# Optimization experiments

Measured on AMD Instinct MI355X. Metric: run time of the kernel, lower is better.

Reference implementation:

```python
import jax, jax.numpy as jnp
import numpy as np

DIM = 2048
NUM_HEADS = 16
HEAD_DIM = DIM // NUM_HEADS
FF_MULT = 2
ROPE_BASE = 10000.0
EPS = 1e-6


def _rmsnorm(x, g):
    return x * jax.lax.rsqrt(jnp.mean(x * x, axis=-1, keepdims=True) + EPS) * g


def _rope_tables(seq_len):
    half = HEAD_DIM // 2
    inv_freq = 1.0 / (ROPE_BASE ** (2.0 * jnp.arange(half, dtype=jnp.float32) / HEAD_DIM))
    angles = jnp.arange(seq_len, dtype=jnp.float32)[:, None] * inv_freq[None, :]  # (S, half)
    return jnp.cos(angles), jnp.sin(angles)


def _apply_rope(x, cos, sin):
    # x: (B, H, S, D); cos/sin: (S, D/2). Interleaved pairs (RoFormer form).
    x_even = x[..., 0::2]
    x_odd = x[..., 1::2]
    c = cos[None, None].astype(x.dtype)
    s = sin[None, None].astype(x.dtype)
    rot_even = x_even * c - x_odd * s
    rot_odd = x_odd * c + x_even * s
    return jnp.stack([rot_even, rot_odd], axis=-1).reshape(x.shape)


def setup_inputs() -> dict:
    key = jax.random.key(0)
    ks = jax.random.split(key, 7)
    B, S = 2, 2048
    scale = 1.0 / np.sqrt(DIM)
    return {
        "x": jax.random.normal(ks[0], (B, S, DIM), dtype=jnp.float32),
        "w_qkv": jax.random.normal(ks[1], (DIM, 3 * DIM), dtype=jnp.float32) * scale,
        "w_out": jax.random.normal(ks[2], (DIM, DIM), dtype=jnp.float32) * scale,
        "w_fc": jax.random.normal(ks[3], (DIM, DIM * FF_MULT), dtype=jnp.float32) * scale,
        "w_proj": jax.random.normal(ks[4], (DIM * FF_MULT, DIM), dtype=jnp.float32) / np.sqrt(DIM * FF_MULT),
        "g_in": jnp.ones((DIM,), dtype=jnp.float32),
        "g_ff": jnp.ones((DIM,), dtype=jnp.float32),
    }


def reference(x, w_qkv, w_out, w_fc, w_proj, g_in, g_ff):
    B, S, D = x.shape
    # --- attention branch ---
    h = _rmsnorm(x, g_in)
    qkv = h @ w_qkv  # (B, S, 3D)
    q, k, v = jnp.split(qkv, 3, axis=-1)
    def heads(t):
        return t.reshape(B, S, NUM_HEADS, HEAD_DIM).transpose(0, 2, 1, 3)
    q, k, v = heads(q), heads(k), heads(v)  # (B, H, S, Dh)
    cos, sin = _rope_tables(S)
    q = _apply_rope(q, cos, sin)
    k = _apply_rope(k, cos, sin)
    scores = jnp.einsum("bhqd,bhkd->bhqk", q, k) / jnp.asarray(np.sqrt(HEAD_DIM), x.dtype)
    causal = jnp.tril(jnp.ones((S, S), dtype=bool))
    scores = jnp.where(causal[None, None], scores, jnp.asarray(-jnp.inf, scores.dtype))
    attn = jax.nn.softmax(scores, axis=-1)
    out = jnp.einsum("bhqk,bhkd->bhqd", attn, v)  # (B, H, S, Dh)
    out = out.transpose(0, 2, 1, 3).reshape(B, S, D)
    x = x + out @ w_out
    # --- feed-forward branch ---
    h = _rmsnorm(x, g_ff)
    x = x + jax.nn.gelu(h @ w_fc) @ w_proj
    return x


if __name__ == "__main__":
    inp = setup_inputs()
    y = reference(**inp)
    print(y.shape, y.dtype)
```

## Files before the change

kernel.cpp:

```cpp
#include <hip/hip_runtime.h>
#include <math.h>

typedef __bf16 bf16x8 __attribute__((ext_vector_type(8)));
typedef __bf16 bf16x4 __attribute__((ext_vector_type(4)));
typedef __bf16 bf16x2 __attribute__((ext_vector_type(2)));
typedef float  f32x4  __attribute__((ext_vector_type(4)));

#define DEV __device__ __forceinline__

DEV void gload16(const void* g, void* l) {
  __builtin_amdgcn_global_load_lds(
      (const __attribute__((address_space(1))) void*)g,
      (__attribute__((address_space(3))) void*)l, 16, 0, 0);
}

__global__ __launch_bounds__(256) void transpose_cvt(
    const float* __restrict__ in, __bf16* __restrict__ outT, int R, int C) {
  __shared__ float t[64][65];
  const int c0 = blockIdx.x * 64, r0 = blockIdx.y * 64;
  const int tid = threadIdx.x;
#pragma unroll
  for (int i = 0; i < 4; i++) {
    int r = (tid >> 4) + i * 16;
    int cf = tid & 15;
    float4 v = *(const float4*)(in + (size_t)(r0 + r) * C + c0 + cf * 4);
    t[r][cf * 4 + 0] = v.x; t[r][cf * 4 + 1] = v.y;
    t[r][cf * 4 + 2] = v.z; t[r][cf * 4 + 3] = v.w;
  }
  __syncthreads();
#pragma unroll
  for (int i = 0; i < 2; i++) {
    int c = (tid >> 3) + i * 32;
    int r8 = tid & 7;
    bf16x8 ov;
#pragma unroll
    for (int k = 0; k < 8; k++) ov[k] = (__bf16)t[r8 * 8 + k][c];
    *(bf16x8*)(outT + (size_t)(c0 + c) * R + r0 + r8 * 8) = ov;
  }
}

__global__ __launch_bounds__(256) void rmsnorm_kernel(
    const float* __restrict__ x, const float* __restrict__ g, __bf16* __restrict__ out) {
  const int r = blockIdx.x, t = threadIdx.x;
  const float4* xr = (const float4*)(x + (size_t)r * 2048);
  float4 a = xr[2 * t], b = xr[2 * t + 1];
  float ss = a.x * a.x + a.y * a.y + a.z * a.z + a.w * a.w +
             b.x * b.x + b.y * b.y + b.z * b.z + b.w * b.w;
#pragma unroll
  for (int mk = 1; mk < 64; mk <<= 1) ss += __shfl_xor(ss, mk);
  __shared__ float red[4];
  if ((t & 63) == 0) red[t >> 6] = ss;
  __syncthreads();
  const float sc = rsqrtf((red[0] + red[1] + red[2] + red[3]) * (1.0f / 2048.0f) + 1e-6f);
  const float4* gr = (const float4*)g;
  float4 ga = gr[2 * t], gb = gr[2 * t + 1];
  bf16x8 ov;
  ov[0] = (__bf16)(a.x * sc * ga.x); ov[1] = (__bf16)(a.y * sc * ga.y);
  ov[2] = (__bf16)(a.z * sc * ga.z); ov[3] = (__bf16)(a.w * sc * ga.w);
  ov[4] = (__bf16)(b.x * sc * gb.x); ov[5] = (__bf16)(b.y * sc * gb.y);
  ov[6] = (__bf16)(b.z * sc * gb.z); ov[7] = (__bf16)(b.w * sc * gb.w);
  *(bf16x8*)(out + (size_t)r * 2048 + t * 8) = ov;
}

template <int EPI>
__global__ __launch_bounds__(256) void gemm_bt(
    const __bf16* __restrict__ A, const __bf16* __restrict__ BT,
    void* __restrict__ Cout, const float* __restrict__ res, int M, int N, int K) {
  __shared__ char lds[32768];
  char* As = lds;
  char* Bs = lds + 16384;
  const int tid = threadIdx.x;
  const int lane = tid & 63;
  const int bn = blockIdx.x, bm = blockIdx.y;
  const int wm = tid >> 7, wn = (tid >> 6) & 1;

  f32x4 acc[4][4];
#pragma unroll
  for (int i = 0; i < 4; i++)
#pragma unroll
    for (int j = 0; j < 4; j++) acc[i][j] = (f32x4){0.f, 0.f, 0.f, 0.f};

  const size_t strideA = (size_t)K * 2;
  const char* ga[4];
  const char* gb[4];
#pragma unroll
  for (int t = 0; t < 4; t++) {
    int gg = t * 256 + tid;
    int row = gg >> 3, slot = gg & 7;
    ga[t] = (const char*)A + (size_t)(bm * 128 + row) * strideA + ((slot ^ (row & 7)) << 4);
    gb[t] = (const char*)BT + (size_t)(bn * 128 + row) * strideA + ((slot ^ (row & 7)) << 4);
  }

  for (int k0 = 0; k0 < K; k0 += 64) {
    __syncthreads();
#pragma unroll
    for (int t = 0; t < 4; t++) {
      int gg = t * 256 + tid;
      gload16(ga[t], As + gg * 16);
      gload16(gb[t], Bs + gg * 16);
      ga[t] += 128;
      gb[t] += 128;
    }
    __syncthreads();
#pragma unroll
    for (int kk = 0; kk < 2; kk++) {
      bf16x8 a[4], b[4];
      const int c16 = kk * 4 + (lane >> 4);
#pragma unroll
      for (int i = 0; i < 4; i++) {
        int ra = wm * 64 + i * 16 + (lane & 15);
        a[i] = *(const bf16x8*)(As + ra * 128 + ((c16 ^ (ra & 7)) << 4));
        int rb = wn * 64 + i * 16 + (lane & 15);
        b[i] = *(const bf16x8*)(Bs + rb * 128 + ((c16 ^ (rb & 7)) << 4));
      }
#pragma unroll
      for (int i = 0; i < 4; i++)
#pragma unroll
        for (int j = 0; j < 4; j++)
          acc[i][j] = __builtin_amdgcn_mfma_f32_16x16x32_bf16(a[i], b[j], acc[i][j], 0, 0, 0);
    }
  }

#pragma unroll
  for (int i = 0; i < 4; i++)
#pragma unroll
    for (int j = 0; j < 4; j++)
#pragma unroll
      for (int r = 0; r < 4; r++) {
        int row = bm * 128 + wm * 64 + i * 16 + ((lane >> 4) << 2) + r;
        int col = bn * 128 + wn * 64 + j * 16 + (lane & 15);
        size_t idx = (size_t)row * N + col;
        float v = acc[i][j][r];
        if (EPI == 0) {
          ((__bf16*)Cout)[idx] = (__bf16)v;
        } else if (EPI == 1) {
          ((float*)Cout)[idx] = v + res[idx];
        } else {
          float u = 0.7978845608028654f * (v + 0.044715f * v * v * v);
          ((__bf16*)Cout)[idx] = (__bf16)(0.5f * v * (1.0f + tanhf(u)));
        }
      }
}

__global__ __launch_bounds__(256, 6) void gemm_qkv(
    const __bf16* __restrict__ A, const __bf16* __restrict__ BT,
    __bf16* __restrict__ qr, __bf16* __restrict__ kr, __bf16* __restrict__ vt,
    int K) {
  __shared__ char lds[32768];
  char* As = lds;
  char* Bs = lds + 16384;
  const int tid = threadIdx.x;
  const int lane = tid & 63;
  const int bn = blockIdx.x, bm = blockIdx.y;
  const int wm = tid >> 7, wn = (tid >> 6) & 1;

  f32x4 acc[4][4];
#pragma unroll
  for (int i = 0; i < 4; i++)
#pragma unroll
    for (int j = 0; j < 4; j++) acc[i][j] = (f32x4){0.f, 0.f, 0.f, 0.f};

  const size_t strideA = (size_t)K * 2;
  const char* ga[4];
  const char* gb[4];
#pragma unroll
  for (int t = 0; t < 4; t++) {
    int gg = t * 256 + tid;
    int row = gg >> 3, slot = gg & 7;
    ga[t] = (const char*)A + (size_t)(bm * 128 + row) * strideA + ((slot ^ (row & 7)) << 4);
    gb[t] = (const char*)BT + (size_t)(bn * 128 + row) * strideA + ((slot ^ (row & 7)) << 4);
  }

  for (int k0 = 0; k0 < K; k0 += 64) {
    __syncthreads();
#pragma unroll
    for (int t = 0; t < 4; t++) {
      int gg = t * 256 + tid;
      gload16(ga[t], As + gg * 16);
      gload16(gb[t], Bs + gg * 16);
      ga[t] += 128;
      gb[t] += 128;
    }
    __syncthreads();
#pragma unroll
    for (int kk = 0; kk < 2; kk++) {
      bf16x8 a[4], b[4];
      const int c16 = kk * 4 + (lane >> 4);
#pragma unroll
      for (int i = 0; i < 4; i++) {
        int ra = wm * 64 + i * 16 + (lane & 15);
        a[i] = *(const bf16x8*)(As + ra * 128 + ((c16 ^ (ra & 7)) << 4));
        int rb = wn * 64 + i * 16 + (lane & 15);
        b[i] = *(const bf16x8*)(Bs + rb * 128 + ((c16 ^ (rb & 7)) << 4));
      }
#pragma unroll
      for (int i = 0; i < 4; i++)
#pragma unroll
        for (int j = 0; j < 4; j++)
          acc[i][j] = __builtin_amdgcn_mfma_f32_16x16x32_bf16(a[i], b[j], acc[i][j], 0, 0, 0);
    }
  }

  const int colbase = bn * 128 + wn * 64;
  if (bn < 32) {
#pragma unroll
    for (int j = 0; j < 4; j++) {
      int col = colbase + j * 16 + (lane & 15);
      int isK = col >> 11;
      int hh = (col >> 7) & 15, d = col & 127;
      float invr = exp2f(-0.20762050593045952f * (float)(d >> 1)) *
                   0.15915494309189535f;
      __bf16* dst = isK ? kr : qr;
#pragma unroll
      for (int i = 0; i < 4; i++)
#pragma unroll
        for (int r = 0; r < 4; r++) {
          int row = bm * 128 + wm * 64 + i * 16 + ((lane >> 4) << 2) + r;
          int bb = row >> 11, srel = row & 2047;
          float me = acc[i][j][r];
          float pv = __shfl_xor(me, 1);
          if (!(lane & 1)) {
            float ar = (float)srel * invr;
            ar = ar - floorf(ar);
            float cs = __builtin_amdgcn_cosf(ar);
            float sn = __builtin_amdgcn_sinf(ar);
            bf16x2 pk;
            pk[0] = (__bf16)(me * cs - pv * sn);
            pk[1] = (__bf16)(pv * cs + me * sn);
            *(bf16x2*)(dst + ((size_t)((bb * 16 + hh) * 2048 + srel)) * 128 + d) = pk;
          }
        }
    }
  } else {
#pragma unroll
    for (int i = 0; i < 4; i++)
#pragma unroll
      for (int j = 0; j < 4; j++) {
        int col = colbase + j * 16 + (lane & 15) - 4096;
        int hh = col >> 7, d = col & 127;
        int row0 = bm * 128 + wm * 64 + i * 16 + ((lane >> 4) << 2);
        int bb = row0 >> 11, srel = row0 & 2047;
        bf16x4 pk;
#pragma unroll
        for (int r = 0; r < 4; r++) pk[r] = (__bf16)acc[i][j][r];
        *(bf16x4*)(vt + ((size_t)((bb * 16 + hh) * 128 + d)) * 2048 + srel) = pk;
      }
  }
}

#define MMQ(IB, JB, AR, BR)                                                   \
  __builtin_amdgcn_s_setprio(1);                                              \
  _Pragma("unroll") for (int i = 0; i < 4; i++)                               \
      _Pragma("unroll") for (int j = 0; j < 2; j++)                           \
          _Pragma("unroll") for (int kk = 0; kk < 2; kk++)                    \
              acc[(IB)*4 + i][(JB)*2 + j] =                                   \
      __builtin_amdgcn_mfma_f32_16x16x32_bf16(                                \
          AR[i][kk], BR[j][kk], acc[(IB)*4 + i][(JB)*2 + j], 0, 0, 0);        \
  __builtin_amdgcn_s_setprio(0);

template <int EPI>
__global__ __launch_bounds__(512, 2) void gemm256(
    const __bf16* __restrict__ A, const __bf16* __restrict__ BT,
    void* __restrict__ Cout, const float* __restrict__ res, int M, int N, int K) {
  __shared__ char lds[131072];
  const int tid = threadIdx.x, lane = tid & 63, w = tid >> 6;
  const int wm = w >> 2, wn = w & 3;
  const int bn = blockIdx.x, bm = blockIdx.y;

  f32x4 acc[8][4];
#pragma unroll
  for (int i = 0; i < 8; i++)
#pragma unroll
    for (int j = 0; j < 4; j++) acc[i][j] = (f32x4){0.f, 0.f, 0.f, 0.f};

  const size_t strideA = (size_t)K * 2;
  const int r0 = tid >> 3, s0 = tid & 7;
  const int r1 = r0 + 64;
  const char* Ab0 = (const char*)A + (size_t)(bm * 256) * strideA;
  const char* Bb0 = (const char*)BT + (size_t)(bn * 256) * strideA;

  auto stage = [&](int isB, int h, int kt, int buf) {
    const char* g = (isB ? Bb0 : Ab0) + (size_t)(h * 128) * strideA + (size_t)kt * 128;
    char* d = lds + isB * 65536 + buf * 32768 + h * 16384;
    gload16(g + (size_t)r0 * strideA + ((s0 ^ (r0 & 7)) << 4), d + tid * 16);
    gload16(g + (size_t)r1 * strideA + ((s0 ^ (r1 & 7)) << 4), d + (tid + 512) * 16);
  };
  auto ldA = [&](bf16x8 (&a)[4][2], int buf, int bank) {
    const char* base = lds + buf * 32768 + wm * 16384;
#pragma unroll
    for (int i = 0; i < 4; i++)
#pragma unroll
      for (int kk = 0; kk < 2; kk++) {
        int rl = bank * 64 + i * 16 + (lane & 15);
        int c16 = kk * 4 + (lane >> 4);
        a[i][kk] = *(const bf16x8*)(base + rl * 128 + ((c16 ^ (rl & 7)) << 4));
      }
  };
  auto ldB = [&](bf16x8 (&b)[2][2], int buf, int jb) {
    const char* base = lds + 65536 + buf * 32768 + (wn >> 1) * 16384;
#pragma unroll
    for (int j = 0; j < 2; j++)
#pragma unroll
      for (int kk = 0; kk < 2; kk++) {
        int rl = (wn & 1) * 64 + jb * 32 + j * 16 + (lane & 15);
        int c16 = kk * 4 + (lane >> 4);
        b[j][kk] = *(const bf16x8*)(base + rl * 128 + ((c16 ^ (rl & 7)) << 4));
      }
  };

  const int NT = K >> 6;
  stage(1, 0, 0, 0); stage(1, 1, 0, 0); stage(0, 0, 0, 0); stage(0, 1, 0, 0);
  stage(1, 0, 1, 1); stage(1, 1, 1, 1); stage(0, 0, 1, 1); stage(0, 1, 1, 1);
  asm volatile("s_waitcnt vmcnt(6)" ::: "memory");
  __builtin_amdgcn_s_barrier();

  bf16x8 a[4][2], b0[2][2], b1[2][2];
  for (int it = 0; it < (NT >> 1); ++it) {
    const int e = 2 * it;
    const int ep = (e + 2 < NT) ? e + 2 : NT - 1;
    const int op = (e + 3 < NT) ? e + 3 : NT - 1;
    ldA(a, 0, 0); ldB(b0, 0, 0);
    __builtin_amdgcn_s_barrier();
    MMQ(0, 0, a, b0);
    __builtin_amdgcn_s_barrier();
    ldB(b1, 0, 1);
    __builtin_amdgcn_s_barrier();
    MMQ(0, 1, a, b1);
    __builtin_amdgcn_s_barrier();
    ldA(a, 0, 1); stage(1, 0, ep, 0);
    __builtin_amdgcn_s_barrier();
    MMQ(1, 1, a, b1);
    __builtin_amdgcn_s_barrier();
    stage(1, 1, ep, 0);
    asm volatile("s_waitcnt vmcnt(4)" ::: "memory");
    __builtin_amdgcn_s_barrier();
    MMQ(1, 0, a, b0);
    __builtin_amdgcn_s_barrier();
    ldA(a, 1, 0); ldB(b0, 1, 0); stage(0, 0, ep, 0);
    __builtin_amdgcn_s_barrier();
    MMQ(0, 0, a, b0);
    __builtin_amdgcn_s_barrier();
    ldB(b1, 1, 1); stage(0, 1, ep, 0);
    __builtin_amdgcn_s_barrier();
    MMQ(0, 1, a, b1);
    __builtin_amdgcn_s_barrier();
    ldA(a, 1, 1); stage(1, 0, op, 1);
    __builtin_amdgcn_s_barrier();
    MMQ(1, 1, a, b1);
    __builtin_amdgcn_s_barrier();
    stage(1, 1, op, 1); stage(0, 0, op, 1); stage(0, 1, op, 1);
    asm volatile("s_waitcnt vmcnt(6)" ::: "memory");
    __builtin_amdgcn_s_barrier();
    MMQ(1, 0, a, b0);
    __builtin_amdgcn_s_barrier();
  }
  asm volatile("s_waitcnt vmcnt(0)" ::: "memory");

#pragma unroll
  for (int i = 0; i < 8; i++)
#pragma unroll
    for (int j = 0; j < 4; j++)
#pragma unroll
      for (int r = 0; r < 4; r++) {
        int row = bm * 256 + wm * 128 + i * 16 + ((lane >> 4) << 2) + r;
        int col = bn * 256 + wn * 64 + j * 16 + (lane & 15);
        size_t idx = (size_t)row * N + col;
        float v = acc[i][j][r];
        if (EPI == 0) {
          ((__bf16*)Cout)[idx] = (__bf16)v;
        } else if (EPI == 1) {
          ((float*)Cout)[idx] = v + res[idx];
        } else {
          float u = 0.7978845608028654f * (v + 0.044715f * v * v * v);
          ((__bf16*)Cout)[idx] = (__bf16)(0.5f * v * (1.0f + tanhf(u)));
        }
      }
}

__global__ __launch_bounds__(512) void flash_attn(
    const __bf16* __restrict__ qg, const __bf16* __restrict__ kg,
    const __bf16* __restrict__ vtg, __bf16* __restrict__ og) {
  __shared__ char lds[81920];
  const int tid = threadIdx.x, lane = tid & 63, w = tid >> 6;
  const int h = blockIdx.y, b = blockIdx.z;
  const int bh = b * 16 + h;
  const __bf16* qb = qg + (size_t)bh * 2048 * 128;
  const char* kbb = (const char*)(kg + (size_t)bh * 2048 * 128);
  const char* vbb = (const char*)(vtg + (size_t)bh * 128 * 2048);
  char* Pw = lds + 65536 + w * 2048;

  const char* gK[2];
  const char* gV[2];
#pragma unroll
  for (int t = 0; t < 2; t++) {
    int gg = t * 512 + tid;
    int rk = gg >> 4, sk = gg & 15;
    gK[t] = kbb + rk * 256 + ((sk ^ (rk & 15)) << 4);
    int rv = gg >> 3, sv = gg & 7;
    gV[t] = vbb + rv * 4096 + ((sv ^ (rv & 7)) << 4);
  }

  const float SL2E = 0.08838834764831845f * 1.4426950408889634f;

  auto stageKV = [&](int kt, int buf) {
#pragma unroll
    for (int t = 0; t < 2; t++) {
      int gg = t * 512 + tid;
      gload16(gK[t] + (size_t)kt * 16384, lds + buf * 16384 + gg * 16);
      gload16(gV[t] + (size_t)kt * 128, lds + 32768 + buf * 16384 + gg * 16);
    }
  };

  auto run_qtile = [&](int qt) {
    const int qrow0 = qt * 128 + w * 16;
    bf16x8 qf[4];
#pragma unroll
    for (int c = 0; c < 4; c++) {
      bf16x8 raw = *(const bf16x8*)(qb + (size_t)(qrow0 + (lane & 15)) * 128 +
                                    c * 32 + ((lane >> 4) << 3));
#pragma unroll
      for (int e = 0; e < 8; e++) qf[c][e] = (__bf16)((float)raw[e] * SL2E);
    }
    float m[4], lsp[4];
    f32x4 o[8];
#pragma unroll
    for (int r = 0; r < 4; r++) { m[r] = -__builtin_inff(); lsp[r] = 0.f; }
#pragma unroll
    for (int n = 0; n < 8; n++) o[n] = (f32x4){0.f, 0.f, 0.f, 0.f};

    const int NKT = 2 * qt + 2;
    stageKV(0, 0);

    for (int kt = 0; kt < NKT; kt++) {
      const int cur = kt & 1;
      const char* Ks = lds + cur * 16384;
      const char* Vs = lds + 32768 + cur * 16384;
      if (kt < NKT - 1) {
        stageKV(kt + 1, cur ^ 1);
        asm volatile("s_waitcnt vmcnt(4)" ::: "memory");
      } else {
        asm volatile("s_waitcnt vmcnt(0)" ::: "memory");
      }
      __builtin_amdgcn_s_barrier();

      f32x4 s[4];
      __builtin_amdgcn_s_setprio(1);
#pragma unroll
      for (int n = 0; n < 4; n++) {
        s[n] = (f32x4){0.f, 0.f, 0.f, 0.f};
#pragma unroll
        for (int c = 0; c < 4; c++) {
          int krow = n * 16 + (lane & 15);
          int c16 = c * 4 + (lane >> 4);
          bf16x8 kf = *(const bf16x8*)(Ks + krow * 256 + ((c16 ^ (krow & 15)) << 4));
          s[n] = __builtin_amdgcn_mfma_f32_16x16x32_bf16(qf[c], kf, s[n], 0, 0, 0);
        }
      }
      __builtin_amdgcn_s_setprio(0);

      if (kt * 64 + 63 > qrow0) {
#pragma unroll
        for (int r = 0; r < 4; r++) {
          const int qrow = qrow0 + ((lane >> 4) << 2) + r;
#pragma unroll
          for (int n = 0; n < 4; n++) {
            int col = kt * 64 + n * 16 + (lane & 15);
            if (col > qrow) s[n][r] = -__builtin_inff();
          }
        }
      }

      float tmx[4];
#pragma unroll
      for (int r = 0; r < 4; r++)
        tmx[r] = fmaxf(fmaxf(s[0][r], s[1][r]), fmaxf(s[2][r], s[3][r]));
      bool hot = (tmx[0] > m[0] + 8.f) | (tmx[1] > m[1] + 8.f) |
                 (tmx[2] > m[2] + 8.f) | (tmx[3] > m[3] + 8.f);
      if (__any(hot)) {
        float fc[4];
#pragma unroll
        for (int r = 0; r < 4; r++) {
          float gmx = tmx[r];
#pragma unroll
          for (int mk = 1; mk < 16; mk <<= 1) gmx = fmaxf(gmx, __shfl_xor(gmx, mk));
          float nm = fmaxf(m[r], gmx);
          fc[r] = __builtin_amdgcn_exp2f(m[r] - nm);
          m[r] = nm;
          lsp[r] *= fc[r];
        }
#pragma unroll
        for (int n = 0; n < 8; n++) {
          o[n][0] *= fc[0]; o[n][1] *= fc[1]; o[n][2] *= fc[2]; o[n][3] *= fc[3];
        }
      }

      float p[4][4];
#pragma unroll
      for (int r = 0; r < 4; r++) {
        float sum = 0.f;
#pragma unroll
        for (int n = 0; n < 4; n++) {
          float pv = __builtin_amdgcn_exp2f(s[n][r] - m[r]);
          p[n][r] = pv;
          sum += pv;
        }
        lsp[r] += sum;
      }

#pragma unroll
      for (int n = 0; n < 4; n++)
#pragma unroll
        for (int r = 0; r < 4; r++) {
          int prow = ((lane >> 4) << 2) + r;
          int col = n * 16 + (lane & 15);
          int ch = col >> 3;
          *(__bf16*)(Pw + prow * 128 + ((ch ^ (prow & 7)) << 4) + ((col & 7) << 1)) =
              (__bf16)p[n][r];
        }

      __builtin_amdgcn_s_setprio(1);
#pragma unroll
      for (int kk = 0; kk < 2; kk++) {
        int prow = lane & 15;
        int pc = kk * 4 + (lane >> 4);
        bf16x8 pf = *(const bf16x8*)(Pw + prow * 128 + ((pc ^ (prow & 7)) << 4));
#pragma unroll
        for (int n = 0; n < 8; n++) {
          int vr = n * 16 + (lane & 15);
          bf16x8 vf = *(const bf16x8*)(Vs + vr * 128 + ((pc ^ (vr & 7)) << 4));
          o[n] = __builtin_amdgcn_mfma_f32_16x16x32_bf16(pf, vf, o[n], 0, 0, 0);
        }
      }
      __builtin_amdgcn_s_setprio(0);
      __builtin_amdgcn_s_barrier();
    }

    float inv[4];
#pragma unroll
    for (int r = 0; r < 4; r++) {
      float ls = lsp[r];
#pragma unroll
      for (int mk = 1; mk < 16; mk <<= 1) ls += __shfl_xor(ls, mk);
      inv[r] = 1.0f / ls;
    }
#pragma unroll
    for (int n = 0; n < 8; n++)
#pragma unroll
      for (int r = 0; r < 4; r++) {
        int qrow = qrow0 + ((lane >> 4) << 2) + r;
        og[(size_t)(b * 2048 + qrow) * 2048 + h * 128 + n * 16 + (lane & 15)] =
            (__bf16)(o[n][r] * inv[r]);
      }
  };

  run_qtile(15 - (int)blockIdx.x);
  run_qtile((int)blockIdx.x);
}

extern "C" void kernel_launch(void* const* d_in, const int* in_sizes, int n_in,
                              void* d_out, int out_size, void* d_ws, size_t ws_size,
                              hipStream_t stream) {
  const float* x = (const float*)d_in[0];
  const float* w_qkv = (const float*)d_in[1];
  const float* w_out = (const float*)d_in[2];
  const float* w_fc = (const float*)d_in[3];
  const float* w_proj = (const float*)d_in[4];
  const float* g_in = (const float*)d_in[5];
  const float* g_ff = (const float*)d_in[6];
  float* out = (float*)d_out;
  char* ws = (char*)d_ws;

  constexpr size_t O_WQKV = 0;
  constexpr size_t O_WOUT = 25165824;
  constexpr size_t O_WFC = 33554432;
  constexpr size_t O_WPROJ = 50331648;
  constexpr size_t O_H = 67108864;
  constexpr size_t O_QKV = 83886080;
  constexpr size_t O_Q = 134217728;
  constexpr size_t O_K = 150994944;
  constexpr size_t O_VT = 167772160;
  constexpr size_t O_ATTN = 185597952;
  constexpr size_t O_X1 = 202375168;

  __bf16* wqkvT = (__bf16*)(ws + O_WQKV);
  __bf16* woutT = (__bf16*)(ws + O_WOUT);
  __bf16* wfcT = (__bf16*)(ws + O_WFC);
  __bf16* wprojT = (__bf16*)(ws + O_WPROJ);
  __bf16* h = (__bf16*)(ws + O_H);
  __bf16* fcact = (__bf16*)(ws + O_QKV);
  __bf16* qr = (__bf16*)(ws + O_Q);
  __bf16* kr = (__bf16*)(ws + O_K);
  __bf16* vt = (__bf16*)(ws + O_VT);
  __bf16* attn = (__bf16*)(ws + O_ATTN);
  float* x1 = (float*)(ws + O_X1);

  transpose_cvt<<<dim3(96, 32), 256, 0, stream>>>(w_qkv, wqkvT, 2048, 6144);
  transpose_cvt<<<dim3(32, 32), 256, 0, stream>>>(w_out, woutT, 2048, 2048);
  transpose_cvt<<<dim3(64, 32), 256, 0, stream>>>(w_fc, wfcT, 2048, 4096);
  transpose_cvt<<<dim3(32, 64), 256, 0, stream>>>(w_proj, wprojT, 4096, 2048);

  rmsnorm_kernel<<<4096, 256, 0, stream>>>(x, g_in, h);
  gemm_qkv<<<dim3(48, 32), 256, 0, stream>>>(h, wqkvT, qr, kr, vt, 2048);
  flash_attn<<<dim3(8, 16, 2), 512, 0, stream>>>(qr, kr, vt, attn);
  gemm_bt<1><<<dim3(16, 32), 256, 0, stream>>>(attn, woutT, (void*)x1, x, 4096, 2048, 2048);
  rmsnorm_kernel<<<4096, 256, 0, stream>>>(x1, g_ff, h);
  gemm256<2><<<dim3(16, 16), 512, 0, stream>>>(h, wfcT, (void*)fcact, nullptr, 4096, 4096, 2048);
  gemm_bt<1><<<dim3(16, 32), 256, 0, stream>>>(fcact, wprojT, (void*)out, x1, 4096, 2048, 4096);
}
```

Measured before the change: 460.4 us.

## Merge weight transposes into one launch and shrink attention P buffer

Combines the four weight transpose/convert launches into a single grid that dispatches on block index, which removes launch overhead and tail gaps between the launches. In flash attention, the per-warp P staging buffer is halved by writing and reading P in 32-column halves inside the kk loop, with a new XOR swizzle. This cuts LDS from 80KB to 72KB, and a launch_bounds occupancy hint is added to try to fit more blocks per CU. The cost is interleaving LDS writes with the MFMA loop and possible register pressure from the occupancy hint.

```diff
diff --git a/kernel.cpp b/kernel.cpp
--- a/kernel.cpp
+++ b/kernel.cpp
@@ -14,10 +14,30 @@
       (__attribute__((address_space(3))) void*)l, 16, 0, 0);
 }
 
-__global__ __launch_bounds__(256) void transpose_cvt(
-    const float* __restrict__ in, __bf16* __restrict__ outT, int R, int C) {
+__global__ __launch_bounds__(256) void transpose_cvt_all(
+    const float* __restrict__ w_qkv, const float* __restrict__ w_out,
+    const float* __restrict__ w_fc, const float* __restrict__ w_proj,
+    __bf16* __restrict__ o_qkv, __bf16* __restrict__ o_out,
+    __bf16* __restrict__ o_fc, __bf16* __restrict__ o_proj) {
+  const int bid = blockIdx.x;
+  const float* in;
+  __bf16* outT;
+  int R, C, bx, by;
+  if (bid < 3072) {
+    in = w_qkv; outT = o_qkv; R = 2048; C = 6144;
+    bx = bid % 96; by = bid / 96;
+  } else if (bid < 4096) {
+    in = w_out; outT = o_out; R = 2048; C = 2048;
+    int l = bid - 3072; bx = l & 31; by = l >> 5;
+  } else if (bid < 6144) {
+    in = w_fc; outT = o_fc; R = 2048; C = 4096;
+    int l = bid - 4096; bx = l & 63; by = l >> 6;
+  } else {
+    in = w_proj; outT = o_proj; R = 4096; C = 2048;
+    int l = bid - 6144; bx = l & 31; by = l >> 5;
+  }
   __shared__ float t[64][65];
-  const int c0 = blockIdx.x * 64, r0 = blockIdx.y * 64;
+  const int c0 = bx * 64, r0 = by * 64;
   const int tid = threadIdx.x;
 #pragma unroll
   for (int i = 0; i < 4; i++) {
@@ -377,17 +397,17 @@
       }
 }
 
-__global__ __launch_bounds__(512) void flash_attn(
+__global__ __launch_bounds__(512, 4) void flash_attn(
     const __bf16* __restrict__ qg, const __bf16* __restrict__ kg,
     const __bf16* __restrict__ vtg, __bf16* __restrict__ og) {
-  __shared__ char lds[81920];
+  __shared__ char lds[73728];
   const int tid = threadIdx.x, lane = tid & 63, w = tid >> 6;
   const int h = blockIdx.y, b = blockIdx.z;
   const int bh = b * 16 + h;
   const __bf16* qb = qg + (size_t)bh * 2048 * 128;
   const char* kbb = (const char*)(kg + (size_t)bh * 2048 * 128);
   const char* vbb = (const char*)(vtg + (size_t)bh * 128 * 2048);
-  char* Pw = lds + 65536 + w * 2048;
+  char* Pw = lds + 65536 + w * 1024;
 
   const char* gK[2];
   const char* gV[2];
@@ -507,26 +527,26 @@
         lsp[r] += sum;
       }
 
-#pragma unroll
-      for (int n = 0; n < 4; n++)
-#pragma unroll
-        for (int r = 0; r < 4; r++) {
-          int prow = ((lane >> 4) << 2) + r;
-          int col = n * 16 + (lane & 15);
-          int ch = col >> 3;
-          *(__bf16*)(Pw + prow * 128 + ((ch ^ (prow & 7)) << 4) + ((col & 7) << 1)) =
-              (__bf16)p[n][r];
-        }
-
       __builtin_amdgcn_s_setprio(1);
 #pragma unroll
       for (int kk = 0; kk < 2; kk++) {
+#pragma unroll
+        for (int n2 = 0; n2 < 2; n2++)
+#pragma unroll
+          for (int r = 0; r < 4; r++) {
+            int prow = ((lane >> 4) << 2) + r;
+            int col = n2 * 16 + (lane & 15);
+            int sch = (col >> 3) ^ (prow & 3) ^ ((prow >> 2) & 3);
+            *(__bf16*)(Pw + prow * 64 + (sch << 4) + ((col & 7) << 1)) =
+                (__bf16)p[kk * 2 + n2][r];
+          }
         int prow = lane & 15;
-        int pc = kk * 4 + (lane >> 4);
-        bf16x8 pf = *(const bf16x8*)(Pw + prow * 128 + ((pc ^ (prow & 7)) << 4));
+        int sch = (lane >> 4) ^ (prow & 3) ^ ((prow >> 2) & 3);
+        bf16x8 pf = *(const bf16x8*)(Pw + prow * 64 + (sch << 4));
 #pragma unroll
         for (int n = 0; n < 8; n++) {
           int vr = n * 16 + (lane & 15);
+          int pc = kk * 4 + (lane >> 4);
           bf16x8 vf = *(const bf16x8*)(Vs + vr * 128 + ((pc ^ (vr & 7)) << 4));
           o[n] = __builtin_amdgcn_mfma_f32_16x16x32_bf16(pf, vf, o[n], 0, 0, 0);
         }
@@ -594,11 +614,8 @@
   __bf16* attn = (__bf16*)(ws + O_ATTN);
   float* x1 = (float*)(ws + O_X1);
 
-  transpose_cvt<<<dim3(96, 32), 256, 0, stream>>>(w_qkv, wqkvT, 2048, 6144);
-  transpose_cvt<<<dim3(32, 32), 256, 0, stream>>>(w_out, woutT, 2048, 2048);
-  transpose_cvt<<<dim3(64, 32), 256, 0, stream>>>(w_fc, wfcT, 2048, 4096);
-  transpose_cvt<<<dim3(32, 64), 256, 0, stream>>>(w_proj, wprojT, 4096, 2048);
-
+  transpose_cvt_all<<<8192, 256, 0, stream>>>(w_qkv, w_out, w_fc, w_proj,
+                                              wqkvT, woutT, wfcT, wprojT);
   rmsnorm_kernel<<<4096, 256, 0, stream>>>(x, g_in, h);
   gemm_qkv<<<dim3(48, 32), 256, 0, stream>>>(h, wqkvT, qr, kr, vt, 2048);
   flash_attn<<<dim3(8, 16, 2), 512, 0, stream>>>(qr, kr, vt, attn);
```

After: 494.5 us. +7.4%, slower.
